# Kernel optimization log

Measured on AMD Instinct MI355X. Metric: run time of the kernel, lower is better.

Reference implementation:

```python
import jax, jax.numpy as jnp
import numpy as np

B, T, D_MODEL = 4, 4096, 512
HEADS, BUCKET_SIZE, N_HASHES = 8, 64, 4
DIM_HEAD = D_MODEL // HEADS  # 64
D_FFN = 2048
N_BUCKETS = T // BUCKET_SIZE  # 64
SELF_ATTN_VALUE = -5e4  # reformer TOKEN_SELF_ATTN_VALUE


def setup_inputs() -> dict:
    key = jax.random.key(0)
    ks = jax.random.split(key, 16)
    s = 0.02
    return {
        'x': jax.random.normal(ks[0], (B, T, D_MODEL), jnp.float32),
        'rotations': jax.random.normal(ks[1], (DIM_HEAD, N_HASHES, N_BUCKETS // 2), jnp.float32),
        'w_qk': jax.random.normal(ks[2], (D_MODEL, D_MODEL), jnp.float32) * s,
        'w_v': jax.random.normal(ks[3], (D_MODEL, D_MODEL), jnp.float32) * s,
        'w_out': jax.random.normal(ks[4], (D_MODEL, D_MODEL), jnp.float32) * s,
        'b_out': jnp.zeros((D_MODEL,), jnp.float32),
        'ln1_g': jnp.ones((D_MODEL,), jnp.float32),
        'ln1_b': jnp.zeros((D_MODEL,), jnp.float32),
        'w1': jax.random.normal(ks[5], (D_FFN, D_MODEL), jnp.float32) * s,
        'b1': jnp.zeros((D_FFN,), jnp.float32),
        'w2': jax.random.normal(ks[6], (D_MODEL, D_FFN), jnp.float32) * s,
        'b2': jnp.zeros((D_MODEL,), jnp.float32),
        'ln2_g': jnp.ones((D_MODEL,), jnp.float32),
        'ln2_b': jnp.zeros((D_MODEL,), jnp.float32),
    }


def layer_norm(x, g, b, eps=1e-6):
    m = x.mean(-1, keepdims=True)
    v = ((x - m) ** 2).mean(-1, keepdims=True)
    return (x - m) / jnp.sqrt(v + eps) * g + b


def look_one_back(x):
    # concat each chunk with the previous chunk (wrap-around), along in-chunk axis
    prev = jnp.roll(x, 1, axis=1)
    return jnp.concatenate([x, prev], axis=2)


def lsh_attention(qk, v, rotations):
    # qk, v: (bh, t, d) with shared-QK; rotations: (d, n_hashes, n_buckets//2)
    bh, t, d = qk.shape
    # --- hash: random rotations, argmax over [R, -R] ---
    rot = jnp.einsum('btf,fhi->bhti', qk, rotations)
    rot = jnp.concatenate([rot, -rot], axis=-1)        # (bh, H, t, n_buckets)
    buckets = jnp.argmax(rot, axis=-1)                 # (bh, H, t)
    buckets = buckets + (jnp.arange(N_HASHES) * N_BUCKETS)[None, :, None]
    buckets = buckets.reshape(bh, N_HASHES * t)
    # --- sort by (bucket, position) ---
    ticker = jnp.arange(N_HASHES * t)
    buckets_and_t = t * buckets + (ticker % t)[None, :]
    sticker = jnp.argsort(buckets_and_t, axis=-1)      # stable sort
    undo_sort = jnp.argsort(sticker, axis=-1)
    st = sticker % t                                   # original positions, sorted order
    sqk = jnp.take_along_axis(qk, st[..., None], axis=1)
    sv = jnp.take_along_axis(v, st[..., None], axis=1)
    # --- chunk: n_hashes*n_buckets chunks of bucket_size tokens ---
    n_chunks = N_HASHES * N_BUCKETS
    bq_t = st.reshape(bh, n_chunks, -1)
    bqk = sqk.reshape(bh, n_chunks, -1, d)
    bv = sv.reshape(bh, n_chunks, -1, d)
    bk = bqk / jnp.clip(jnp.linalg.norm(bqk, axis=-1, keepdims=True), 1e-6, None)
    bk = look_one_back(bk)
    bv = look_one_back(bv)
    bkv_t = look_one_back(bq_t)
    # --- local attention within chunk (+ previous chunk) ---
    dots = jnp.einsum('bcid,bcjd->bcij', bqk, bk) * (DIM_HEAD ** -0.5)
    self_mask = bq_t[..., None] == bkv_t[..., None, :]
    dots = jnp.where(self_mask, SELF_ATTN_VALUE, dots)
    logits = jax.nn.logsumexp(dots, axis=-1, keepdims=True)
    probs = jnp.exp(dots - logits)
    bo = jnp.einsum('bcij,bcjd->bcid', probs, bv)
    # --- unsort and combine hash rounds by softmax over round logits ---
    so = bo.reshape(bh, N_HASHES * t, d)
    slogits = logits.reshape(bh, N_HASHES * t)
    o = jnp.take_along_axis(so, undo_sort[..., None], axis=1).reshape(bh, N_HASHES, t, d)
    lg = jnp.take_along_axis(slogits, undo_sort, axis=1).reshape(bh, N_HASHES, t, 1)
    w = jnp.exp(lg - jax.nn.logsumexp(lg, axis=1, keepdims=True))
    return (o * w).sum(axis=1)                         # (bh, t, d)


def reference(x, rotations, w_qk, w_v, w_out, b_out, ln1_g, ln1_b, w1, b1, w2, b2, ln2_g, ln2_b):
    b, t, _ = x.shape
    qk = x @ w_qk.T
    v = x @ w_v.T

    def split_heads(u):
        return u.reshape(b, t, HEADS, DIM_HEAD).transpose(0, 2, 1, 3).reshape(b * HEADS, t, DIM_HEAD)

    attn = lsh_attention(split_heads(qk), split_heads(v), rotations)
    attn = attn.reshape(b, HEADS, t, DIM_HEAD).transpose(0, 2, 1, 3).reshape(b, t, D_MODEL)
    attn = attn @ w_out.T + b_out
    # residual + LN (dropout is identity at inference)
    h = layer_norm(attn + x, ln1_g, ln1_b)
    # position-wise FFN with its own residual + LN
    f = jax.nn.relu(h @ w1.T + b1) @ w2.T + b2
    return layer_norm(f + h, ln2_g, ln2_b)
```

## Files before the change

kernel.cpp:

```cpp
#include <hip/hip_runtime.h>
#include <stdint.h>

typedef unsigned short u16;
typedef __attribute__((ext_vector_type(4))) int   i32x4;
typedef __attribute__((ext_vector_type(4))) float f32x4;

__device__ __forceinline__ u16 f2bf(float x){
  unsigned int u = __float_as_uint(x);
  u += 0x7FFFu + ((u >> 16) & 1u);
  return (u16)(u >> 16);
}
__device__ __forceinline__ float bf2f(u16 h){
  return __uint_as_float(((unsigned int)h) << 16);
}
__device__ __forceinline__ unsigned int cvtpk_bf16(float lo, float hi){
  unsigned int r;
  asm("v_cvt_pk_bf16_f32 %0, %1, %2" : "=v"(r) : "v"(lo), "v"(hi));
  return r;
}
__device__ __forceinline__ f32x4 mfma16(i32x4 a, i32x4 b, f32x4 c){
  asm("v_mfma_f32_16x16x32_bf16 %0, %1, %2, %0" : "+v"(c) : "v"(a), "v"(b));
  return c;
}
__device__ __forceinline__ f32x4 acc_fence(f32x4 c){
  asm volatile("s_nop 7\ns_nop 7" : "+v"(c));
  return c;
}
__device__ __forceinline__ void gl_lds16(const void* g, void* l){
  unsigned long long ga = (unsigned long long)g;
  unsigned int la = (unsigned int)(unsigned long long)l;
  __builtin_amdgcn_global_load_lds((const __attribute__((address_space(1))) void*)ga,
                                   (__attribute__((address_space(3))) void*)la, 16, 0, 0);
}
__device__ __forceinline__ int xcd_swz(int f, int n){
  int chunk = n >> 3;
  return (f & 7) * chunk + (f >> 3);
}
__device__ __forceinline__ unsigned int f2mono(float v){
  unsigned int u = __float_as_uint(v);
  return u ^ ((unsigned int)((int)u >> 31) | 0x80000000u);
}
__device__ __forceinline__ float mono2f(unsigned int mu){
  unsigned int u = (mu & 0x80000000u) ? (mu ^ 0x80000000u) : ~mu;
  return __uint_as_float(u);
}
__device__ __forceinline__ unsigned long long shfl_xor_u64(unsigned long long x, int m){
  int lo = __shfl_xor((int)(unsigned int)(x & 0xFFFFFFFFull), m);
  int hi = __shfl_xor((int)(unsigned int)(x >> 32), m);
  return ((unsigned long long)(unsigned int)hi << 32) | (unsigned int)lo;
}

__global__ __launch_bounds__(256) void k_split(const float* __restrict__ in, u16* __restrict__ hi, u16* __restrict__ lo, int n4){
  int i = blockIdx.x*256 + threadIdx.x;
  if (i >= n4) return;
  float4 v = ((const float4*)in)[i];
  ushort4 h, l;
  h.x=f2bf(v.x); l.x=f2bf(v.x - bf2f(h.x));
  h.y=f2bf(v.y); l.y=f2bf(v.y - bf2f(h.y));
  h.z=f2bf(v.z); l.z=f2bf(v.z - bf2f(h.z));
  h.w=f2bf(v.w); l.w=f2bf(v.w - bf2f(h.w));
  ((ushort4*)hi)[i]=h; ((ushort4*)lo)[i]=l;
}

__global__ __launch_bounds__(256) void k_wprep(
    const float* __restrict__ w_qk, const float* __restrict__ w_v,
    const float* __restrict__ w_out, const float* __restrict__ w1,
    const float* __restrict__ w2, const float* __restrict__ rot,
    u16* __restrict__ wqkh, u16* __restrict__ wqkl,
    u16* __restrict__ wvb, u16* __restrict__ wob,
    u16* __restrict__ w1b, u16* __restrict__ w2b,
    u16* __restrict__ rothi, u16* __restrict__ rotlo)
{
  const int bid = blockIdx.x;
  if (bid >= 2816){
    int i = (bid - 2816)*256 + threadIdx.x;
    int d = i & 63, n = i >> 6;
    float v = rot[d*128 + n];
    u16 h = f2bf(v);
    rothi[i] = h; rotlo[i] = f2bf(v - bf2f(h));
    return;
  }
  const int i = bid*256 + threadIdx.x;
  if (i < 65536){
    float4 v = ((const float4*)w_qk)[i];
    ushort4 h, l;
    h.x=f2bf(v.x); l.x=f2bf(v.x - bf2f(h.x));
    h.y=f2bf(v.y); l.y=f2bf(v.y - bf2f(h.y));
    h.z=f2bf(v.z); l.z=f2bf(v.z - bf2f(h.z));
    h.w=f2bf(v.w); l.w=f2bf(v.w - bf2f(h.w));
    ((ushort4*)wqkh)[i]=h; ((ushort4*)wqkl)[i]=l;
    return;
  }
  const float* src; u16* dst; int j;
  if (i < 131072){ src = w_v;  dst = wvb; j = i - 65536; }
  else if (i < 196608){ src = w_out; dst = wob; j = i - 131072; }
  else if (i < 458752){ src = w1;   dst = w1b; j = i - 196608; }
  else { src = w2; dst = w2b; j = i - 458752; }
  float4 v = ((const float4*)src)[j];
  ushort4 o; o.x=f2bf(v.x); o.y=f2bf(v.y); o.z=f2bf(v.z); o.w=f2bf(v.w);
  ((ushort4*)dst)[j] = o;
}

template<int MODE>
__global__ __launch_bounds__(256) void k_gemm(
    const u16* __restrict__ A0, const u16* __restrict__ B0,
    const float* __restrict__ bias,
    float* __restrict__ Cf, u16* __restrict__ Cb,
    int M, int N, int K)
{
  const int tid = threadIdx.x;
  const int l = tid & 63, w = tid >> 6;
  const int lr = l & 15, lg = l >> 4;
  int flat = blockIdx.y * gridDim.x + blockIdx.x;
  flat = xcd_swz(flat, gridDim.x * gridDim.y);
  const int m0 = (flat / gridDim.x) * 128, n0 = (flat % gridDim.x) * 128;
  const int mbase = (w >> 1) * 64, nbase = (w & 1) * 64;

  __shared__ __align__(16) u16 As[128*64];
  __shared__ __align__(16) u16 Bs[128*64];

  f32x4 zero = {0.f,0.f,0.f,0.f};
  f32x4 acc[4][4];
  #pragma unroll
  for (int i=0;i<4;i++)
    #pragma unroll
    for (int j=0;j<4;j++) acc[i][j] = zero;

  const int row_s = tid >> 3;
  const int c16   = tid & 7;

  for (int k0 = 0; k0 < K; k0 += 64){
    #pragma unroll
    for (int q=0;q<4;q++){
      int ra = q*32 + row_s;
      int cs = c16 ^ (ra & 7);
      gl_lds16(A0 + (size_t)(m0 + ra)*K + k0 + cs*8, (char*)As + q*4096 + tid*16);
      gl_lds16(B0 + (size_t)(n0 + ra)*K + k0 + cs*8, (char*)Bs + q*4096 + tid*16);
    }
    __syncthreads();
    #pragma unroll
    for (int kk=0; kk<64; kk+=32){
      i32x4 af[4], bfr[4];
      #pragma unroll
      for (int mf=0;mf<4;mf++){
        int row = mbase + mf*16 + lr;
        af[mf] = *(const i32x4*)((const char*)As + row*128 + (((kk*2) + (lg*16)) ^ ((row&7)<<4)));
      }
      #pragma unroll
      for (int nf=0;nf<4;nf++){
        int row = nbase + nf*16 + lr;
        bfr[nf] = *(const i32x4*)((const char*)Bs + row*128 + (((kk*2) + (lg*16)) ^ ((row&7)<<4)));
      }
      #pragma unroll
      for (int mf=0;mf<4;mf++)
        #pragma unroll
        for (int nf=0;nf<4;nf++)
          acc[mf][nf] = mfma16(af[mf], bfr[nf], acc[mf][nf]);
    }
    __syncthreads();
  }

  #pragma unroll
  for (int mf=0;mf<4;mf++){
    #pragma unroll
    for (int nf=0;nf<4;nf++){
      f32x4 v = acc_fence(acc[mf][nf]);
      #pragma unroll
      for (int r=0;r<4;r++){
        int m = m0 + mbase + mf*16 + lg*4 + r;
        int n = n0 + nbase + nf*16 + lr;
        float val = v[r];
        if (MODE == 1){
          val += bias[n];
          val = fmaxf(val, 0.f);
          Cb[(size_t)m*N + n] = f2bf(val);
        } else if (MODE == 4){
          val += bias[n];
          Cb[(size_t)m*N + n] = f2bf(val);
        } else {
          int b = m >> 12, t = m & 4095, h = n >> 6, d = n & 63;
          size_t idx = ((((size_t)(b*8 + h)) << 12) + t)*64 + d;
          Cb[idx] = f2bf(val);
        }
      }
    }
  }
}

__global__ __launch_bounds__(256) void k_gemmqk(
    const u16* __restrict__ Ah, const u16* __restrict__ Al,
    const u16* __restrict__ Bh, const u16* __restrict__ Bl,
    const u16* __restrict__ rotH, const u16* __restrict__ rotL,
    u16* __restrict__ qb, u16* __restrict__ qlo, u16* __restrict__ kn,
    int* __restrict__ Bkt)
{
  const int K = 512;
  const int tid = threadIdx.x;
  const int l = tid & 63, w = tid >> 6;
  const int lr = l & 15, lg = l >> 4;
  int flat = blockIdx.y * gridDim.x + blockIdx.x;
  flat = xcd_swz(flat, gridDim.x * gridDim.y);
  const int m0 = (flat >> 2) * 128, n0 = (flat & 3) * 128;
  const int mbase = (w >> 1) * 64, nbase = (w & 1) * 64;

  __shared__ __align__(16) u16 AsH[128*64];
  __shared__ __align__(16) u16 AsL[128*64];
  __shared__ __align__(16) u16 BsH[128*64];
  __shared__ __align__(16) u16 BsL[128*64];

  f32x4 zero = {0.f,0.f,0.f,0.f};
  f32x4 acc[4][4];
  #pragma unroll
  for (int i=0;i<4;i++)
    #pragma unroll
    for (int j=0;j<4;j++) acc[i][j] = zero;

  const int row_s = tid >> 3;
  const int c16   = tid & 7;

  for (int k0 = 0; k0 < K; k0 += 64){
    #pragma unroll
    for (int q=0;q<4;q++){
      int ra = q*32 + row_s;
      int cs = c16 ^ (ra & 7);
      size_t ao = (size_t)(m0 + ra)*K + k0 + cs*8;
      size_t bo = (size_t)(n0 + ra)*K + k0 + cs*8;
      gl_lds16(Ah + ao, (char*)AsH + q*4096 + tid*16);
      gl_lds16(Al + ao, (char*)AsL + q*4096 + tid*16);
      gl_lds16(Bh + bo, (char*)BsH + q*4096 + tid*16);
      gl_lds16(Bl + bo, (char*)BsL + q*4096 + tid*16);
    }
    __syncthreads();
    #pragma unroll
    for (int kk=0; kk<64; kk+=32){
      i32x4 ah[4], al[4], bh2[4], bl2[4];
      #pragma unroll
      for (int mf=0;mf<4;mf++){
        int row = mbase + mf*16 + lr;
        int off = (((kk*2) + (lg*16)) ^ ((row&7)<<4));
        ah[mf] = *(const i32x4*)((const char*)AsH + row*128 + off);
        al[mf] = *(const i32x4*)((const char*)AsL + row*128 + off);
      }
      #pragma unroll
      for (int nf=0;nf<4;nf++){
        int row = nbase + nf*16 + lr;
        int off = (((kk*2) + (lg*16)) ^ ((row&7)<<4));
        bh2[nf] = *(const i32x4*)((const char*)BsH + row*128 + off);
        bl2[nf] = *(const i32x4*)((const char*)BsL + row*128 + off);
      }
      #pragma unroll
      for (int mf=0;mf<4;mf++)
        #pragma unroll
        for (int nf=0;nf<4;nf++){
          acc[mf][nf] = mfma16(ah[mf], bh2[nf], acc[mf][nf]);
          acc[mf][nf] = mfma16(al[mf], bh2[nf], acc[mf][nf]);
          acc[mf][nf] = mfma16(ah[mf], bl2[nf], acc[mf][nf]);
        }
    }
    __syncthreads();
  }

  const int head = (n0 + nbase) >> 6;
  const int b = m0 >> 12;
  const int t0 = (m0 & 4095) + mbase;
  #pragma unroll
  for (int mf=0;mf<4;mf++){
    f32x4 v[4];
    #pragma unroll
    for (int nf=0;nf<4;nf++) v[nf] = acc_fence(acc[mf][nf]);
    #pragma unroll
    for (int r=0;r<4;r++){
      float ss = 0.f;
      #pragma unroll
      for (int nf=0;nf<4;nf++) ss += v[nf][r]*v[nf][r];
      ss += __shfl_xor(ss, 1); ss += __shfl_xor(ss, 2);
      ss += __shfl_xor(ss, 4); ss += __shfl_xor(ss, 8);
      float scale = 0.18033688f / fmaxf(sqrtf(ss), 1e-6f);
      int t = t0 + mf*16 + lg*4 + r;
      size_t rowb = ((((size_t)(b*8 + head)) << 12) + t) * 64;
      #pragma unroll
      for (int nf=0;nf<4;nf++){
        float val = v[nf][r];
        u16 hbf = f2bf(val);
        size_t idx = rowb + nf*16 + lr;
        qb [idx] = hbf;
        qlo[idx] = f2bf(val - bf2f(hbf));
        kn [idx] = f2bf(val * scale);
      }
    }
  }

  asm volatile("s_waitcnt vmcnt(0)" ::: "memory");
  const size_t qrow0 = (((size_t)(b*8 + head)) << 12) + t0;
  i32x4 qhf[2][4], qlf[2][4];
  #pragma unroll
  for (int ks=0; ks<2; ks++)
    #pragma unroll
    for (int nt=0; nt<4; nt++){
      size_t off = (qrow0 + nt*16 + lr)*64 + ks*32 + lg*8;
      qhf[ks][nt] = *(const i32x4*)(qb + off);
      qlf[ks][nt] = *(const i32x4*)(qlo + off);
    }
  #pragma unroll
  for (int half=0; half<2; half++){
    f32x4 hacc[4][4];
    #pragma unroll
    for (int i=0;i<4;i++)
      #pragma unroll
      for (int j=0;j<4;j++) hacc[i][j] = zero;
    #pragma unroll
    for (int ks=0; ks<2; ks++){
      #pragma unroll
      for (int mf2=0; mf2<4; mf2++){
        int rowr = half*64 + mf2*16 + lr;
        i32x4 rh = *(const i32x4*)(rotH + rowr*64 + ks*32 + lg*8);
        i32x4 rl = *(const i32x4*)(rotL + rowr*64 + ks*32 + lg*8);
        #pragma unroll
        for (int nt=0; nt<4; nt++){
          hacc[mf2][nt] = mfma16(rh, qhf[ks][nt], hacc[mf2][nt]);
          hacc[mf2][nt] = mfma16(rl, qhf[ks][nt], hacc[mf2][nt]);
          hacc[mf2][nt] = mfma16(rh, qlf[ks][nt], hacc[mf2][nt]);
        }
      }
    }
    #pragma unroll
    for (int g=0; g<2; g++){
      int hh = half*2 + g;
      #pragma unroll
      for (int nt=0; nt<4; nt++){
        f32x4 v0 = acc_fence(hacc[2*g][nt]);
        f32x4 v1 = acc_fence(hacc[2*g+1][nt]);
        unsigned long long kmax = 0, kmin = 0;
        #pragma unroll
        for (int r = 0; r < 4; r++){
          int j0 = lg*4 + r, j1 = 16 + lg*4 + r;
          unsigned int mu0 = f2mono(v0[r]), mu1 = f2mono(v1[r]);
          unsigned long long a = ((unsigned long long)mu0 << 32) | (unsigned int)(31 - j0);
          unsigned long long b2 = ((unsigned long long)mu1 << 32) | (unsigned int)(31 - j1);
          if (a > kmax) kmax = a;
          if (b2 > kmax) kmax = b2;
          unsigned long long c2 = ((unsigned long long)(~mu0) << 32) | (unsigned int)(31 - j0);
          unsigned long long d2 = ((unsigned long long)(~mu1) << 32) | (unsigned int)(31 - j1);
          if (c2 > kmin) kmin = c2;
          if (d2 > kmin) kmin = d2;
        }
        #pragma unroll
        for (int msk = 16; msk < 64; msk <<= 1){
          unsigned long long o1 = shfl_xor_u64(kmax, msk); if (o1 > kmax) kmax = o1;
          unsigned long long o2 = shfl_xor_u64(kmin, msk); if (o2 > kmin) kmin = o2;
        }
        if (lg == 0){
          float vmax = mono2f((unsigned int)(kmax >> 32));
          int jmax = 31 - (int)(kmax & 0xFFFFFFFFull);
          float vmin = mono2f(~(unsigned int)(kmin >> 32));
          int jmin = 31 - (int)(kmin & 0xFFFFFFFFull);
          int bucket = (vmax >= -vmin) ? jmax : 32 + jmin;
          int t = t0 + nt*16 + lr;
          Bkt[((size_t)((b*8 + head)*4 + hh) << 12) + t] = bucket;
        }
      }
    }
  }
}

__global__ __launch_bounds__(64) void k_sort(const int* __restrict__ buckets, int* __restrict__ st){
  const int grp = blockIdx.x;
  const int t = threadIdx.x;
  __shared__ int bkL[4096];
  __shared__ int hist[64][65];
  __shared__ int tot[64];
  const size_t gbase = ((size_t)grp) << 12;
  for (int i=0;i<64;i++)
    bkL[i*64 + t] = buckets[gbase + i*64 + t];
  #pragma unroll
  for (int b=0;b<64;b++) hist[t][b] = 0;
  __syncthreads();
  for (int i=0;i<64;i++){
    int b = bkL[t*64 + i];
    hist[t][b]++;
  }
  __syncthreads();
  { int run = 0;
    for (int tt=0; tt<64; tt++){ int v = hist[tt][t]; hist[tt][t] = run; run += v; }
    tot[t] = run; }
  __syncthreads();
  { int v = tot[t]; int incl = v;
    #pragma unroll
    for (int d=1; d<64; d<<=1){ int n = __shfl_up(incl, d, 64); if (t >= d) incl += n; }
    tot[t] = incl - v; }
  __syncthreads();
  const size_t obase = (((size_t)(grp>>2)) << 14) + ((size_t)(grp&3) << 12);
  for (int i=0;i<64;i++){
    int e = t*64 + i;
    int b = bkL[e];
    int dest = tot[b] + hist[t][b];
    hist[t][b]++;
    st[obase + dest] = e;
  }
}

__global__ __launch_bounds__(256, 5) void k_attn(
    const u16* __restrict__ qb, const u16* __restrict__ kn, const u16* __restrict__ vB,
    const int* __restrict__ st, float* __restrict__ lgt_out, u16* __restrict__ bo)
{
  int flat = blockIdx.y * gridDim.x + blockIdx.x;
  flat = xcd_swz(flat, gridDim.x * gridDim.y);
  const int c = flat & 255, bh = flat >> 8;
  const int rnd = c >> 6;
  const int cprev = (c + 255) & 255;
  const int tid = threadIdx.x;
  const int l = tid & 63, w = tid >> 6, lr = l & 15, lg = l >> 4;

  __shared__ __align__(16) u16 Ks[128*64];
  __shared__ __align__(16) u16 Vt[64*128];

  const size_t stbase = ((size_t)bh) << 14;
  const size_t kvbase = ((size_t)bh) << 12;

  {
    const int rsub = l >> 3, c8 = l & 7;
    #pragma unroll
    for (int q2 = 0; q2 < 4; q2++){
      int row = w*32 + q2*8 + rsub;
      int cc = (row < 64) ? c : cprev;
      int pos = st[stbase + (cc << 6) + (row & 63)];
      int cs = c8 ^ (row & 7);
      gl_lds16(kn + (kvbase + pos)*64 + cs*8,
               (char*)Ks + (w*4 + q2)*1024 + l*16);
    }
  }

  const int pos_q16 = st[stbase + (c << 6) + (w*16 + lr)];
  i32x4 qf[2];
  #pragma unroll
  for (int ks = 0; ks < 2; ks++)
    qf[ks] = *(const i32x4*)(qb + (kvbase + pos_q16)*64 + ks*32 + lg*8);

  {
    const int pp = tid & 63, db = tid >> 6;
    const int q5 = pp & 15;
    const int K0 = (pp >> 4)*32 + 16*((q5 >> 1) & 1) + 4*(q5 >> 2) + 2*(q5 & 1);
    int cc0 = (K0 < 64) ? c : cprev;
    int p0 = st[stbase + (cc0 << 6) + (K0 & 63)];
    int p1 = st[stbase + (cc0 << 6) + ((K0 + 1) & 63)];
    const u16* r0 = vB + (kvbase + p0)*64 + db*16;
    const u16* r1 = vB + (kvbase + p1)*64 + db*16;
    uint4 a0 = *(const uint4*)r0, a1 = *(const uint4*)(r0 + 8);
    uint4 b0 = *(const uint4*)r1, b1 = *(const uint4*)(r1 + 8);
    uint av[8] = {a0.x,a0.y,a0.z,a0.w,a1.x,a1.y,a1.z,a1.w};
    uint bv[8] = {b0.x,b0.y,b0.z,b0.w,b1.x,b1.y,b1.z,b1.w};
    #pragma unroll
    for (int dd = 0; dd < 16; dd++){
      uint lo = (av[dd>>1] >> ((dd&1)*16)) & 0xFFFFu;
      uint hi = (bv[dd>>1] >> ((dd&1)*16)) & 0xFFFFu;
      int row = db*16 + dd;
      *(uint*)((char*)Vt + row*256 + ((pp*4) ^ ((row & 7) << 5))) = lo | (hi << 16);
    }
  }
  const bool bdry = (c & 63) == 0;
  int pkprev[4][4];
  if (bdry){
    #pragma unroll
    for (int nf2=0; nf2<4; nf2++)
      #pragma unroll
      for (int r=0;r<4;r++)
        pkprev[nf2][r] = st[stbase + (cprev << 6) + nf2*16 + lg*4 + r];
  }
  __syncthreads();

  f32x4 zero = {0.f,0.f,0.f,0.f};
  f32x4 s[8];
  #pragma unroll
  for (int i=0;i<8;i++) s[i] = zero;
  __builtin_amdgcn_s_setprio(1);
  #pragma unroll
  for (int ks = 0; ks < 2; ks++){
    #pragma unroll
    for (int nf = 0; nf < 8; nf++){
      int row = nf*16 + lr;
      i32x4 kf = *(const i32x4*)((const char*)Ks + row*128 + ((ks*64 + lg*16) ^ ((row&7)<<4)));
      s[nf] = mfma16(kf, qf[ks], s[nf]);
    }
  }
  __builtin_amdgcn_s_setprio(0);

  float p[8][4];
  float sum = 0.f;
  #pragma unroll
  for (int nf=0;nf<8;nf++){
    f32x4 t = acc_fence(s[nf]);
    #pragma unroll
    for (int r=0;r<4;r++){
      float e = __builtin_amdgcn_exp2f(t[r]);
      if (nf == w && (lg*4 + r) == lr) e = 0.f;
      if (nf >= 4 && bdry && pkprev[nf-4][r] == pos_q16) e = 0.f;
      p[nf][r] = e;
      sum += e;
    }
  }
  sum += __shfl_xor(sum, 16);
  sum += __shfl_xor(sum, 32);
  float lv = logf(sum);
  float inv = 1.f / sum;
  if (l < 16)
    lgt_out[((((size_t)bh) << 12) + pos_q16)*4 + rnd] = lv;

  i32x4 pa[4];
  #pragma unroll
  for (int ks=0;ks<4;ks++){
    uint w0 = cvtpk_bf16(p[2*ks][0],   p[2*ks][1]);
    uint w1 = cvtpk_bf16(p[2*ks][2],   p[2*ks][3]);
    uint w2 = cvtpk_bf16(p[2*ks+1][0], p[2*ks+1][1]);
    uint w3 = cvtpk_bf16(p[2*ks+1][2], p[2*ks+1][3]);
    i32x4 t = {(int)w0,(int)w1,(int)w2,(int)w3};
    pa[ks] = t;
  }

  f32x4 o[4];
  #pragma unroll
  for (int i=0;i<4;i++) o[i] = zero;
  __builtin_amdgcn_s_setprio(1);
  #pragma unroll
  for (int ks=0;ks<4;ks++){
    #pragma unroll
    for (int nf=0;nf<4;nf++){
      int row = nf*16 + lr;
      i32x4 vf = *(const i32x4*)((const char*)Vt + row*256 + ((ks*64 + lg*16) ^ ((row & 7) << 5)));
      o[nf] = mfma16(pa[ks], vf, o[nf]);
    }
  }
  __builtin_amdgcn_s_setprio(0);
  float invq[4]; int posq[4];
  #pragma unroll
  for (int r=0;r<4;r++){
    invq[r] = __shfl(inv, lg*4 + r, 64);
    posq[r] = __shfl(pos_q16, lg*4 + r, 64);
  }
  #pragma unroll
  for (int nf=0;nf<4;nf++){
    f32x4 ov = acc_fence(o[nf]);
    #pragma unroll
    for (int r=0;r<4;r++){
      bo[((((size_t)bh << 12) + posq[r]))*256 + rnd*64 + nf*16 + lr] = f2bf(ov[r] * invq[r]);
    }
  }
}

__global__ __launch_bounds__(256) void k_combine(const u16* __restrict__ bo, const float* __restrict__ lgt,
                                                 u16* __restrict__ attn){
  const int wid = blockIdx.x * 4 + (threadIdx.x >> 6);
  const int l = threadIdx.x & 63;
  const int bh = wid >> 12, t = wid & 4095;
  const size_t tb = (((size_t)bh) << 12) + t;
  float4 lg4 = *(const float4*)(lgt + tb*4);
  float m = fmaxf(fmaxf(lg4.x,lg4.y), fmaxf(lg4.z,lg4.w));
  float w0 = __expf(lg4.x-m), w1 = __expf(lg4.y-m), w2 = __expf(lg4.z-m), w3 = __expf(lg4.w-m);
  float inv = 1.f / (w0+w1+w2+w3);
  const u16* bp = bo + tb*256;
  float o = w0 * bf2f(bp[l]) + w1 * bf2f(bp[64+l]) + w2 * bf2f(bp[128+l]) + w3 * bf2f(bp[192+l]);
  o *= inv;
  int b = bh >> 3, h = bh & 7;
  attn[((((size_t)b) << 12) + t) * 512 + h*64 + l] = f2bf(o);
}

template<int RESF>
__global__ __launch_bounds__(256) void k_ln(const u16* __restrict__ a,
                                            const float* __restrict__ resf, const u16* __restrict__ resb,
                                            const float* __restrict__ g, const float* __restrict__ bb,
                                            float* __restrict__ of, u16* __restrict__ ob){
  const int row = blockIdx.x*4 + (threadIdx.x >> 6);
  const int l = threadIdx.x & 63;
  const size_t base = (size_t)row*512 + l*8;
  uint4 aa = *(const uint4*)(a + base);
  uint aw[4] = {aa.x, aa.y, aa.z, aa.w};
  float av[8];
  #pragma unroll
  for (int j=0;j<4;j++){
    av[2*j]   = bf2f((u16)(aw[j] & 0xFFFF));
    av[2*j+1] = bf2f((u16)(aw[j] >> 16));
  }
  float rv[8];
  if (RESF){
    float4 r0 = *(const float4*)(resf + base);
    float4 r1 = *(const float4*)(resf + base + 4);
    rv[0]=r0.x; rv[1]=r0.y; rv[2]=r0.z; rv[3]=r0.w;
    rv[4]=r1.x; rv[5]=r1.y; rv[6]=r1.z; rv[7]=r1.w;
  } else {
    uint4 rr = *(const uint4*)(resb + base);
    uint rw[4] = {rr.x, rr.y, rr.z, rr.w};
    #pragma unroll
    for (int j=0;j<4;j++){
      rv[2*j]   = bf2f((u16)(rw[j] & 0xFFFF));
      rv[2*j+1] = bf2f((u16)(rw[j] >> 16));
    }
  }
  float v[8];
  #pragma unroll
  for (int j=0;j<8;j++) v[j] = av[j] + rv[j];
  float sum = 0.f;
  #pragma unroll
  for (int j=0;j<8;j++) sum += v[j];
  #pragma unroll
  for (int msk=1; msk<64; msk<<=1) sum += __shfl_xor(sum, msk);
  float mean = sum * (1.f/512.f);
  float ss = 0.f;
  #pragma unroll
  for (int j=0;j<8;j++){ float d = v[j]-mean; ss += d*d; }
  #pragma unroll
  for (int msk=1; msk<64; msk<<=1) ss += __shfl_xor(ss, msk);
  float rstd = rsqrtf(ss * (1.f/512.f) + 1e-6f);
  float4 g0 = *(const float4*)(g + l*8),  g1 = *(const float4*)(g + l*8 + 4);
  float4 b0 = *(const float4*)(bb + l*8), b1 = *(const float4*)(bb + l*8 + 4);
  float gv[8] = {g0.x,g0.y,g0.z,g0.w,g1.x,g1.y,g1.z,g1.w};
  float bv[8] = {b0.x,b0.y,b0.z,b0.w,b1.x,b1.y,b1.z,b1.w};
  float y[8];
  #pragma unroll
  for (int j=0;j<8;j++) y[j] = (v[j]-mean)*rstd*gv[j] + bv[j];
  if (RESF){
    #pragma unroll
    for (int j=0;j<8;j++) ob[base+j] = f2bf(y[j]);
  } else {
    #pragma unroll
    for (int j=0;j<8;j++) of[base+j] = y[j];
  }
}

extern "C" void kernel_launch(void* const* d_in, const int* in_sizes, int n_in,
                              void* d_out, int out_size, void* d_ws, size_t ws_size,
                              hipStream_t stream) {
  const float* x     = (const float*)d_in[0];
  const float* rot   = (const float*)d_in[1];
  const float* w_qk  = (const float*)d_in[2];
  const float* w_v   = (const float*)d_in[3];
  const float* w_out = (const float*)d_in[4];
  const float* b_out = (const float*)d_in[5];
  const float* ln1_g = (const float*)d_in[6];
  const float* ln1_b = (const float*)d_in[7];
  const float* w1    = (const float*)d_in[8];
  const float* b1    = (const float*)d_in[9];
  const float* w2    = (const float*)d_in[10];
  const float* b2    = (const float*)d_in[11];
  const float* ln2_g = (const float*)d_in[12];
  const float* ln2_b = (const float*)d_in[13];
  float* out = (float*)d_out;

  char* p = (char*)d_ws;
  u16*   xh   = (u16*)(p);
  u16*   xl   = (u16*)(p + 16777216);
  u16*   wqkh = (u16*)(p + 33554432);
  u16*   wqkl = (u16*)(p + 34078720);
  u16*   wvb  = (u16*)(p + 34603008);
  u16*   wob  = (u16*)(p + 35127296);
  u16*   w1b  = (u16*)(p + 35651584);
  u16*   w2b  = (u16*)(p + 37748736);
  u16*   qbuf = (u16*)(p + 39845888);
  u16*   knb  = (u16*)(p + 56623104);
  u16*   vb   = (u16*)(p + 73400320);
  int*   bkt  = (int*)(p + 90177536);
  int*   stb  = (int*)(p + 92274688);
  float* lgt  = (float*)(p + 94371840);
  u16*   bo   = (u16*)(p + 96468992);
  u16*   qlo   = bo;
  u16*   rothi = (u16*)(p + 96468992 + 16777216);
  u16*   rotlo = (u16*)(p + 96468992 + 16777216 + 16384);
  u16*   attnc = xl;
  u16*   projb = qbuf;
  u16*   fb    = xl;
  u16*   hb    = xh;
  u16*   hid   = bo;

  k_split<<<8192, 256, 0, stream>>>(x, xh, xl, 16384*512/4);
  k_wprep<<<2848, 256, 0, stream>>>(w_qk, w_v, w_out, w1, w2, rot,
                                    wqkh, wqkl, wvb, wob, w1b, w2b, rothi, rotlo);
  k_gemmqk<<<dim3(4,128), 256, 0, stream>>>(xh, xl, wqkh, wqkl, rothi, rotlo,
                                            qbuf, qlo, knb, bkt);
  k_gemm<3><<<dim3(4,128), 256, 0, stream>>>(xh, wvb, nullptr, nullptr, vb, 16384, 512, 512);
  k_sort<<<128, 64, 0, stream>>>(bkt, stb);
  k_attn<<<dim3(256,32), 256, 0, stream>>>(qbuf, knb, vb, stb, lgt, bo);
  k_combine<<<32768, 256, 0, stream>>>(bo, lgt, attnc);
  k_gemm<4><<<dim3(4,128), 256, 0, stream>>>(attnc, wob, b_out, nullptr, projb, 16384, 512, 512);
  k_ln<1><<<4096, 256, 0, stream>>>(projb, x, nullptr, ln1_g, ln1_b, nullptr, hb);
  k_gemm<1><<<dim3(16,128), 256, 0, stream>>>(hb, w1b, b1, nullptr, hid, 16384, 2048, 512);
  k_gemm<4><<<dim3(4,128), 256, 0, stream>>>(hid, w2b, b2, nullptr, fb, 16384, 512, 2048);
  k_ln<0><<<4096, 256, 0, stream>>>(fb, nullptr, hb, ln2_g, ln2_b, out, nullptr);
}
```

Baseline: 286.0 us.

## Split LSH hashing out of QK GEMM epilogue into separate kernel

Moves the rotation-hash MFMA and argmax step out of the QK projection GEMM epilogue into a new k_hash2 kernel. The new kernel stages the rotation matrix in swizzled LDS and has each wave hash 16 rows. The aim is to cut register pressure and the tail latency of the GEMM epilogue, which had to re-read its own freshly written q output from global memory. The cost is an extra kernel launch and a second read of the q hi/lo buffers from global memory.

```diff
diff --git a/kernel.cpp b/kernel.cpp
--- a/kernel.cpp
+++ b/kernel.cpp
@@ -190,9 +190,7 @@
 __global__ __launch_bounds__(256) void k_gemmqk(
     const u16* __restrict__ Ah, const u16* __restrict__ Al,
     const u16* __restrict__ Bh, const u16* __restrict__ Bl,
-    const u16* __restrict__ rotH, const u16* __restrict__ rotL,
-    u16* __restrict__ qb, u16* __restrict__ qlo, u16* __restrict__ kn,
-    int* __restrict__ Bkt)
+    u16* __restrict__ qb, u16* __restrict__ qlo, u16* __restrict__ kn)
 {
   const int K = 512;
   const int tid = threadIdx.x;
@@ -260,9 +258,7 @@
     __syncthreads();
   }
 
-  const int head = (n0 + nbase) >> 6;
-  const int b = m0 >> 12;
-  const int t0 = (m0 & 4095) + mbase;
+  const int hh = (n0 + nbase) >> 6;
   #pragma unroll
   for (int mf=0;mf<4;mf++){
     f32x4 v[4];
@@ -276,8 +272,9 @@
       ss += __shfl_xor(ss, 1); ss += __shfl_xor(ss, 2);
       ss += __shfl_xor(ss, 4); ss += __shfl_xor(ss, 8);
       float scale = 0.18033688f / fmaxf(sqrtf(ss), 1e-6f);
-      int t = t0 + mf*16 + lg*4 + r;
-      size_t rowb = ((((size_t)(b*8 + head)) << 12) + t) * 64;
+      int m = m0 + mbase + mf*16 + lg*4 + r;
+      int b = m >> 12, t = m & 4095;
+      size_t rowb = ((((size_t)(b*8 + hh)) << 12) + t) * 64;
       #pragma unroll
       for (int nf=0;nf<4;nf++){
         float val = v[nf][r];
@@ -289,76 +286,86 @@
       }
     }
   }
-
-  asm volatile("s_waitcnt vmcnt(0)" ::: "memory");
-  const size_t qrow0 = (((size_t)(b*8 + head)) << 12) + t0;
-  i32x4 qhf[2][4], qlf[2][4];
-  #pragma unroll
-  for (int ks=0; ks<2; ks++)
-    #pragma unroll
-    for (int nt=0; nt<4; nt++){
-      size_t off = (qrow0 + nt*16 + lr)*64 + ks*32 + lg*8;
-      qhf[ks][nt] = *(const i32x4*)(qb + off);
-      qlf[ks][nt] = *(const i32x4*)(qlo + off);
-    }
-  #pragma unroll
-  for (int half=0; half<2; half++){
-    f32x4 hacc[4][4];
-    #pragma unroll
-    for (int i=0;i<4;i++)
-      #pragma unroll
-      for (int j=0;j<4;j++) hacc[i][j] = zero;
-    #pragma unroll
-    for (int ks=0; ks<2; ks++){
-      #pragma unroll
-      for (int mf2=0; mf2<4; mf2++){
-        int rowr = half*64 + mf2*16 + lr;
-        i32x4 rh = *(const i32x4*)(rotH + rowr*64 + ks*32 + lg*8);
-        i32x4 rl = *(const i32x4*)(rotL + rowr*64 + ks*32 + lg*8);
-        #pragma unroll
-        for (int nt=0; nt<4; nt++){
-          hacc[mf2][nt] = mfma16(rh, qhf[ks][nt], hacc[mf2][nt]);
-          hacc[mf2][nt] = mfma16(rl, qhf[ks][nt], hacc[mf2][nt]);
-          hacc[mf2][nt] = mfma16(rh, qlf[ks][nt], hacc[mf2][nt]);
-        }
-      }
-    }
-    #pragma unroll
-    for (int g=0; g<2; g++){
-      int hh = half*2 + g;
-      #pragma unroll
-      for (int nt=0; nt<4; nt++){
-        f32x4 v0 = acc_fence(hacc[2*g][nt]);
-        f32x4 v1 = acc_fence(hacc[2*g+1][nt]);
-        unsigned long long kmax = 0, kmin = 0;
-        #pragma unroll
-        for (int r = 0; r < 4; r++){
-          int j0 = lg*4 + r, j1 = 16 + lg*4 + r;
-          unsigned int mu0 = f2mono(v0[r]), mu1 = f2mono(v1[r]);
-          unsigned long long a = ((unsigned long long)mu0 << 32) | (unsigned int)(31 - j0);
-          unsigned long long b2 = ((unsigned long long)mu1 << 32) | (unsigned int)(31 - j1);
-          if (a > kmax) kmax = a;
-          if (b2 > kmax) kmax = b2;
-          unsigned long long c2 = ((unsigned long long)(~mu0) << 32) | (unsigned int)(31 - j0);
-          unsigned long long d2 = ((unsigned long long)(~mu1) << 32) | (unsigned int)(31 - j1);
-          if (c2 > kmin) kmin = c2;
-          if (d2 > kmin) kmin = d2;
-        }
-        #pragma unroll
-        for (int msk = 16; msk < 64; msk <<= 1){
-          unsigned long long o1 = shfl_xor_u64(kmax, msk); if (o1 > kmax) kmax = o1;
-          unsigned long long o2 = shfl_xor_u64(kmin, msk); if (o2 > kmin) kmin = o2;
-        }
-        if (lg == 0){
-          float vmax = mono2f((unsigned int)(kmax >> 32));
-          int jmax = 31 - (int)(kmax & 0xFFFFFFFFull);
-          float vmin = mono2f(~(unsigned int)(kmin >> 32));
-          int jmin = 31 - (int)(kmin & 0xFFFFFFFFull);
-          int bucket = (vmax >= -vmin) ? jmax : 32 + jmin;
-          int t = t0 + nt*16 + lr;
-          Bkt[((size_t)((b*8 + head)*4 + hh) << 12) + t] = bucket;
-        }
-      }
+}
+
+__global__ __launch_bounds__(256) void k_hash2(
+    const u16* __restrict__ qh, const u16* __restrict__ ql,
+    const u16* __restrict__ rh, const u16* __restrict__ rl,
+    int* __restrict__ bkt)
+{
+  const int tid = threadIdx.x;
+  const int l = tid & 63, w = tid >> 6, lr = l & 15, lg = l >> 4;
+  __shared__ __align__(16) u16 Rh[128*64];
+  __shared__ __align__(16) u16 Rl[128*64];
+  {
+    const int row_s = tid >> 3, c8 = tid & 7;
+    #pragma unroll
+    for (int q = 0; q < 4; q++){
+      int ra = q*32 + row_s;
+      int cs = c8 ^ (ra & 7);
+      gl_lds16(rh + ra*64 + cs*8, (char*)Rh + q*4096 + tid*16);
+      gl_lds16(rl + ra*64 + cs*8, (char*)Rl + q*4096 + tid*16);
+    }
+  }
+  const int blk = xcd_swz(blockIdx.x, gridDim.x);
+  const int qrow = blk*64 + w*16 + lr;
+  const size_t qoff = (size_t)qrow*64;
+  i32x4 qhf[2], qlf[2];
+  qhf[0] = *(const i32x4*)(qh + qoff + lg*8);
+  qhf[1] = *(const i32x4*)(qh + qoff + 32 + lg*8);
+  qlf[0] = *(const i32x4*)(ql + qoff + lg*8);
+  qlf[1] = *(const i32x4*)(ql + qoff + 32 + lg*8);
+  __syncthreads();
+
+  f32x4 zero = {0.f,0.f,0.f,0.f};
+  f32x4 acc[8];
+  #pragma unroll
+  for (int i=0;i<8;i++) acc[i] = zero;
+  #pragma unroll
+  for (int ks = 0; ks < 2; ks++){
+    #pragma unroll
+    for (int nf = 0; nf < 8; nf++){
+      int row = nf*16 + lr;
+      int off = (ks*64 + lg*16) ^ ((row & 7) << 4);
+      i32x4 rhf = *(const i32x4*)((const char*)Rh + row*128 + off);
+      i32x4 rlf = *(const i32x4*)((const char*)Rl + row*128 + off);
+      acc[nf] = mfma16(rhf, qhf[ks], acc[nf]);
+      acc[nf] = mfma16(rlf, qhf[ks], acc[nf]);
+      acc[nf] = mfma16(rhf, qlf[ks], acc[nf]);
+    }
+  }
+
+  const int bh = qrow >> 12, t = qrow & 4095;
+  #pragma unroll
+  for (int hh = 0; hh < 4; hh++){
+    f32x4 v0 = acc_fence(acc[2*hh]);
+    f32x4 v1 = acc_fence(acc[2*hh+1]);
+    unsigned long long kmax = 0, kmin = 0;
+    #pragma unroll
+    for (int r = 0; r < 4; r++){
+      int j0 = lg*4 + r, j1 = 16 + lg*4 + r;
+      unsigned int mu0 = f2mono(v0[r]), mu1 = f2mono(v1[r]);
+      unsigned long long a = ((unsigned long long)mu0 << 32) | (unsigned int)(31 - j0);
+      unsigned long long b = ((unsigned long long)mu1 << 32) | (unsigned int)(31 - j1);
+      if (a > kmax) kmax = a;
+      if (b > kmax) kmax = b;
+      unsigned long long c = ((unsigned long long)(~mu0) << 32) | (unsigned int)(31 - j0);
+      unsigned long long d = ((unsigned long long)(~mu1) << 32) | (unsigned int)(31 - j1);
+      if (c > kmin) kmin = c;
+      if (d > kmin) kmin = d;
+    }
+    #pragma unroll
+    for (int msk = 16; msk < 64; msk <<= 1){
+      unsigned long long o1 = shfl_xor_u64(kmax, msk); if (o1 > kmax) kmax = o1;
+      unsigned long long o2 = shfl_xor_u64(kmin, msk); if (o2 > kmin) kmin = o2;
+    }
+    if (lg == 0){
+      float vmax = mono2f((unsigned int)(kmax >> 32));
+      int jmax = 31 - (int)(kmax & 0xFFFFFFFFull);
+      float vmin = mono2f(~(unsigned int)(kmin >> 32));
+      int jmin = 31 - (int)(kmin & 0xFFFFFFFFull);
+      int bucket = (vmax >= -vmin) ? jmax : 32 + jmin;
+      bkt[((size_t)(bh*4 + hh) << 12) + t] = bucket;
     }
   }
 }
@@ -672,9 +679,9 @@
   k_split<<<8192, 256, 0, stream>>>(x, xh, xl, 16384*512/4);
   k_wprep<<<2848, 256, 0, stream>>>(w_qk, w_v, w_out, w1, w2, rot,
                                     wqkh, wqkl, wvb, wob, w1b, w2b, rothi, rotlo);
-  k_gemmqk<<<dim3(4,128), 256, 0, stream>>>(xh, xl, wqkh, wqkl, rothi, rotlo,
-                                            qbuf, qlo, knb, bkt);
+  k_gemmqk<<<dim3(4,128), 256, 0, stream>>>(xh, xl, wqkh, wqkl, qbuf, qlo, knb);
   k_gemm<3><<<dim3(4,128), 256, 0, stream>>>(xh, wvb, nullptr, nullptr, vb, 16384, 512, 512);
+  k_hash2<<<2048, 256, 0, stream>>>(qbuf, qlo, rothi, rotlo, bkt);
   k_sort<<<128, 64, 0, stream>>>(bkt, stb);
   k_attn<<<dim3(256,32), 256, 0, stream>>>(qbuf, knb, vb, stb, lgt, bo);
   k_combine<<<32768, 256, 0, stream>>>(bo, lgt, attnc);
```

Result: no change. 282.4 us (-1.3%).
